# Performance work log

Hardware: AMD Instinct MI355X
Metric: run time of the kernel (lower is better)

## Reference

```python
import jax, jax.numpy as jnp
import numpy as np

K = 32768   # latent dim of p
CARD = 50   # number of persistence pairs


def setup_inputs() -> dict:
    key = jax.random.key(0)
    k0, k1, k2, k3, k4, k5 = jax.random.split(key, 6)
    p0 = jax.random.normal(k0, (K,), dtype=jnp.float32)
    p1 = jax.random.normal(k1, (K,), dtype=jnp.float32)
    I1 = jax.random.normal(k2, (784, K), dtype=jnp.float32)
    I2 = jax.random.normal(k3, (784, K), dtype=jnp.float32)
    # Cubical persistence indices are stop_gradient int constants in the
    # original (computed host-side via tf.numpy_function); model as inputs.
    inds1 = jax.random.randint(k4, (2 * 2 * CARD,), 0, 28, dtype=jnp.int32)
    inds2 = jax.random.randint(k5, (2 * 2 * CARD,), 0, 28, dtype=jnp.int32)
    return {"p0": p0, "p1": p1, "I1": I1, "I2": I2,
            "inds1": inds1, "inds2": inds2}


def _diagram(img, inds):
    # img: [28,28]; inds: [200] int32 -> 100 (row,col) pairs -> [50,2] diagram
    idx = inds.reshape(-1, 2)
    vals = img[idx[:, 0], idx[:, 1]]
    return vals.reshape(-1, 2)


def reference(p0, p1, I1, I2, inds1, inds2):
    Xp = jnp.reshape(I1 @ p0, (28, 28))
    Yp = jnp.reshape(I2 @ p1, (28, 28))
    dgm1 = _diagram(Xp, inds1)
    dgm2 = _diagram(Yp, inds2)
    return (dgm1, dgm2)
```

## Files before the change

### kernel.cpp

```cpp
#include <hip/hip_runtime.h>

#define KDIM 32768

__global__ __launch_bounds__(512) void cubical_gather_matvec(
    const float* __restrict__ p0, const float* __restrict__ p1,
    const float* __restrict__ I1, const float* __restrict__ I2,
    const int* __restrict__ inds1, const int* __restrict__ inds2,
    float* __restrict__ out)
{
    const int bid = blockIdx.x;
    const float* p;
    const float* I;
    const int* inds;
    int i;
    if (bid < 100) { p = p0; I = I1; inds = inds1; i = bid; }
    else           { p = p1; I = I2; inds = inds2; i = bid - 100; }

    const int r = inds[2 * i];
    const int c = inds[2 * i + 1];
    const float* row = I + (size_t)(r * 28 + c) * KDIM;

    const int tid = threadIdx.x;
    const float4* row4 = (const float4*)row;
    const float4* p4   = (const float4*)p;

    float acc = 0.f;
    #pragma unroll 4
    for (int j = tid; j < KDIM / 4; j += 512) {
        float4 a = row4[j];
        float4 b = p4[j];
        acc += a.x * b.x + a.y * b.y + a.z * b.z + a.w * b.w;
    }

    #pragma unroll
    for (int off = 32; off > 0; off >>= 1)
        acc += __shfl_down(acc, off, 64);

    __shared__ float s[8];
    const int lane = tid & 63;
    const int wid  = tid >> 6;
    if (lane == 0) s[wid] = acc;
    __syncthreads();
    if (tid == 0) {
        float t = 0.f;
        #pragma unroll
        for (int w = 0; w < 8; ++w) t += s[w];
        out[bid] = t;
    }
}

extern "C" void kernel_launch(void* const* d_in, const int* in_sizes, int n_in,
                              void* d_out, int out_size, void* d_ws, size_t ws_size,
                              hipStream_t stream) {
    const float* p0    = (const float*)d_in[0];
    const float* p1    = (const float*)d_in[1];
    const float* I1    = (const float*)d_in[2];
    const float* I2    = (const float*)d_in[3];
    const int*   inds1 = (const int*)d_in[4];
    const int*   inds2 = (const int*)d_in[5];
    float* out = (float*)d_out;

    cubical_gather_matvec<<<200, 512, 0, stream>>>(p0, p1, I1, I2, inds1, inds2, out);
}
```

Baseline: 185.1 us.

## Split K across four blocks per output with atomic accumulation

Each of the 200 gathered dot products is now split into four K-chunks handled by separate 256-thread blocks, giving 800 blocks instead of 200 so more of the GPU's compute units have work and more memory requests are in flight. Partial sums are combined with atomicAdd into the output, which is zeroed first by an extra small kernel launch. The cost is a second launch, atomic traffic, and a summation order that is no longer deterministic.

```diff
diff --git a/kernel.cpp b/kernel.cpp
--- a/kernel.cpp
+++ b/kernel.cpp
@@ -1,51 +1,61 @@
 #include <hip/hip_runtime.h>
 
-#define KDIM 32768
+#define KDIM   32768
+#define NCHUNK 4
+#define CHUNK  (KDIM / NCHUNK)
+#define TPB    256
 
-__global__ __launch_bounds__(512) void cubical_gather_matvec(
+__global__ void zero_out(float* __restrict__ out, int n) {
+    int i = blockIdx.x * blockDim.x + threadIdx.x;
+    if (i < n) out[i] = 0.f;
+}
+
+__global__ __launch_bounds__(TPB) void cubical_gather_matvec_splitk(
     const float* __restrict__ p0, const float* __restrict__ p1,
     const float* __restrict__ I1, const float* __restrict__ I2,
     const int* __restrict__ inds1, const int* __restrict__ inds2,
     float* __restrict__ out)
 {
-    const int bid = blockIdx.x;
+    const int b       = blockIdx.x;
+    const int out_idx = b >> 2;
+    const int chunk   = b & (NCHUNK - 1);
+
     const float* p;
     const float* I;
     const int* inds;
     int i;
-    if (bid < 100) { p = p0; I = I1; inds = inds1; i = bid; }
-    else           { p = p1; I = I2; inds = inds2; i = bid - 100; }
+    if (out_idx < 100) { p = p0; I = I1; inds = inds1; i = out_idx; }
+    else               { p = p1; I = I2; inds = inds2; i = out_idx - 100; }
 
     const int r = inds[2 * i];
     const int c = inds[2 * i + 1];
-    const float* row = I + (size_t)(r * 28 + c) * KDIM;
+    const float* row = I + (size_t)(r * 28 + c) * KDIM + (size_t)chunk * CHUNK;
+    const float* pc  = p + (size_t)chunk * CHUNK;
 
     const int tid = threadIdx.x;
     const float4* row4 = (const float4*)row;
-    const float4* p4   = (const float4*)p;
+    const float4* p4   = (const float4*)pc;
 
     float acc = 0.f;
-    #pragma unroll 4
-    for (int j = tid; j < KDIM / 4; j += 512) {
+    #pragma unroll 8
+    for (int j = tid; j < CHUNK / 4; j += TPB) {
         float4 a = row4[j];
-        float4 b = p4[j];
-        acc += a.x * b.x + a.y * b.y + a.z * b.z + a.w * b.w;
+        float4 v = p4[j];
+        acc += a.x * v.x + a.y * v.y + a.z * v.z + a.w * v.w;
     }
 
     #pragma unroll
     for (int off = 32; off > 0; off >>= 1)
         acc += __shfl_down(acc, off, 64);
 
-    __shared__ float s[8];
+    __shared__ float s[4];
     const int lane = tid & 63;
     const int wid  = tid >> 6;
     if (lane == 0) s[wid] = acc;
     __syncthreads();
     if (tid == 0) {
-        float t = 0.f;
-        #pragma unroll
-        for (int w = 0; w < 8; ++w) t += s[w];
-        out[bid] = t;
+        float t = s[0] + s[1] + s[2] + s[3];
+        atomicAdd(&out[out_idx], t);
     }
 }
 
@@ -60,5 +70,7 @@
     const int*   inds2 = (const int*)d_in[5];
     float* out = (float*)d_out;
 
-    cubical_gather_matvec<<<200, 512, 0, stream>>>(p0, p1, I1, I2, inds1, inds2, out);
+    zero_out<<<1, 256, 0, stream>>>(out, out_size);
+    cubical_gather_matvec_splitk<<<200 * NCHUNK, TPB, 0, stream>>>(
+        p0, p1, I1, I2, inds1, inds2, out);
 }
```

Result: no change. 185.5 us (+0.2%).
